# Optimization experiments

Measured on AMD Instinct MI355X. Metric: run time of the kernel, lower is better.

## Reference

```python
import jax, jax.numpy as jnp
import numpy as np

B, C, H = 2, 32, 64  # batch, concat channels, cube side (H==W==D required by attaxis reshapes)
Ch = C // 2


def _conv3d(x, w, b, pad):
    # conv3d block = Conv3d + bias + ReLU (n=1 conv block)
    y = jax.lax.conv_general_dilated(x, w, (1, 1, 1), [(p, p) for p in pad],
                                     dimension_numbers=('NCDHW', 'OIDHW', 'NCDHW'))
    return jax.nn.relu(y + b[None, :, None, None, None])


def setup_inputs():
    key = jax.random.key(0)
    ks = jax.random.split(key, 16)
    w = lambda k, s: jax.random.normal(k, s, dtype=jnp.float32) * 0.05
    z = lambda n: jnp.zeros((n,), jnp.float32)
    return {
        'x1': jax.random.normal(ks[0], (B, Ch, H, H, H), jnp.float32),
        'x2': jax.random.normal(ks[1], (B, Ch, H, H, H), jnp.float32),
        'w_red': w(ks[2], (1, C, 3, 3, 3)), 'b_red': z(1),
        'w_cx': w(ks[3], (1, 1, 1, 1, H)), 'b_cx': z(1),
        'w_cy': w(ks[4], (1, 1, 1, H, 1)), 'b_cy': z(1),
        'w_cz': w(ks[5], (1, 1, H, 1, 1)), 'b_cz': z(1),
        'w_sp1': w(ks[6], (1, 1, 1, 1, 1)), 'b_sp1': z(1),
        'w_sp3': w(ks[7], (1, 1, 3, 3, 3)), 'b_sp3': z(1),
        'w_sp5a': w(ks[8], (1, 1, 3, 3, 3)), 'b_sp5a': z(1),
        'w_sp5b': w(ks[9], (1, 1, 3, 3, 3)), 'b_sp5b': z(1),
        'w_fus': w(ks[10], (C, 1, 3, 3, 3)), 'b_fus': z(C),
        'w_c1': w(ks[11], (Ch, Ch, 3, 3, 3)), 'b_c1': z(Ch),
        'w_c2': w(ks[12], (Ch, Ch, 3, 3, 3)), 'b_c2': z(Ch),
    }


def _kernal(x, w_cx, b_cx, w_cy, b_cy, w_cz, b_cz,
            w_sp1, b_sp1, w_sp3, b_sp3, w_sp5a, b_sp5a, w_sp5b, b_sp5b):
    b, c, h, ww, d = x.shape
    # xyzaxis: axis-collapsing convs, then attaxis attention over S = h*w tokens
    q = _conv3d(x, w_cx, b_cx, (0, 0, 0))                        # [b,1,h,w,1]
    k = jnp.swapaxes(_conv3d(x, w_cy, b_cy, (0, 0, 0)), 3, 4)    # [b,1,h,d,1]
    v = jnp.swapaxes(_conv3d(x, w_cz, b_cz, (0, 0, 0)), 2, 4)    # [b,1,d,w,1]
    S = h * ww
    Q = q.reshape(b, S, 1)
    K = k.reshape(b, S, 1)
    V = v.reshape(b, S, 1)
    qk = jax.nn.softmax(jnp.einsum('bsc,btc->bst', Q, K), axis=-1)  # [b,S,S]
    xyz = jnp.einsum('bst,btc->bsc', qk, V).reshape(b, 1, h, ww, 1)
    # multi-branch convs + full-tensor att(sp1, sp3, sp5)
    sp1 = _conv3d(x, w_sp1, b_sp1, (0, 0, 0))
    sp3 = _conv3d(x, w_sp3, b_sp3, (1, 1, 1))
    sp5 = _conv3d(_conv3d(x, w_sp5a, b_sp5a, (1, 1, 1)), w_sp5b, b_sp5b, (1, 1, 1))
    attn = jnp.matmul(jax.nn.softmax(jnp.matmul(sp1, sp3), axis=-1), sp5)
    return xyz + attn + x  # xyz broadcasts over last dim


def reference(x1, x2, w_red, b_red, w_cx, b_cx, w_cy, b_cy, w_cz, b_cz,
              w_sp1, b_sp1, w_sp3, b_sp3, w_sp5a, b_sp5a, w_sp5b, b_sp5b,
              w_fus, b_fus, w_c1, b_c1, w_c2, b_c2):
    x = jnp.concatenate([x1, x2], axis=1)                 # [B,C,H,H,H]
    hx = _conv3d(x, w_red, b_red, (1, 1, 1))              # DenseSP.reducePool -> 1 channel
    hx = _kernal(hx, w_cx, b_cx, w_cy, b_cy, w_cz, b_cz,
                 w_sp1, b_sp1, w_sp3, b_sp3, w_sp5a, b_sp5a, w_sp5b, b_sp5b)
    sp = jax.nn.sigmoid(_conv3d(hx, w_fus, b_fus, (1, 1, 1)) + x)  # DenseSP output
    x = sp * x + x
    c = x.shape[1] // 2
    y1 = _conv3d(x[:, :c] + x1, w_c1, b_c1, (1, 1, 1))
    y2 = _conv3d(x[:, c:] + x2, w_c2, b_c2, (1, 1, 1))
    return (y1, y2)
```

## Files before the change

kernel.cpp:

```cpp
#include <hip/hip_runtime.h>

#define DEVFN static __device__ __forceinline__

constexpr int HHH = 262144;
constexpr int HH  = 4096;
constexpr int RP  = 19;

typedef __attribute__((ext_vector_type(8))) short short8;
typedef __attribute__((ext_vector_type(4))) float f32x4;

#define OFF_HX   ((size_t)0)
#define OFF_SP3  (OFF_HX   + 2*(size_t)HHH)
#define OFF_SP5A (OFF_SP3  + 2*(size_t)HHH)
#define OFF_SP5B (OFF_SP5A + 2*(size_t)HHH)
#define OFF_HXO  (OFF_SP5B + 2*(size_t)HHH)
#define OFF_Q    (OFF_HXO  + 2*(size_t)HHH)
#define OFF_K    (OFF_Q    + 2*(size_t)HH)
#define OFF_V    (OFF_K    + 2*(size_t)HH)
#define OFF_XYZ  (OFF_V    + 2*(size_t)HH)
#define OFF_KM   (OFF_XYZ  + 2*(size_t)HH)
#define OFF_Z    (OFF_KM   + 16)
#define OFF_WPRE (OFF_Z    + 32*(size_t)HHH)

DEVFN unsigned short f2bf(float f)
{
    unsigned u = __builtin_bit_cast(unsigned, f);
    u += 0x7fffu + ((u >> 16) & 1u);
    return (unsigned short)(u >> 16);
}

DEVFN void stage1800(const float* __restrict__ src, float* __restrict__ tile,
                     int z0, int y0, int x0, int tid)
{
    for (int i = tid; i < 1800; i += 256) {
        int lz = i / 180;
        int r  = i - lz * 180;
        int ly = r / 18;
        int lx = r - ly * 18;
        int gz = z0 - 1 + lz, gy = y0 - 1 + ly, gx = x0 - 1 + lx;
        float v = 0.f;
        if ((unsigned)(gz | gy | gx) < 64u)
            v = src[(gz * 64 + gy) * 64 + gx];
        tile[(lz * 10 + ly) * RP + lx] = v;
    }
}

DEVFN float4 conv27(const float* __restrict__ tile, int tz, int ty, int txg,
                    const float* __restrict__ wc, float4 acc)
{
#pragma unroll
    for (int dz = 0; dz < 3; ++dz) {
#pragma unroll
        for (int dy = 0; dy < 3; ++dy) {
            const float* row = &tile[((tz + dz) * 10 + (ty + dy)) * RP + txg * 4];
            float p0 = row[0], p1 = row[1], p2 = row[2];
            float p3 = row[3], p4 = row[4], p5 = row[5];
            const float* wr = wc + (dz * 3 + dy) * 3;
            float w0 = wr[0], w1 = wr[1], w2 = wr[2];
            acc.x = fmaf(p0, w0, fmaf(p1, w1, fmaf(p2, w2, acc.x)));
            acc.y = fmaf(p1, w0, fmaf(p2, w1, fmaf(p3, w2, acc.y)));
            acc.z = fmaf(p2, w0, fmaf(p3, w1, fmaf(p4, w2, acc.z)));
            acc.w = fmaf(p3, w0, fmaf(p4, w1, fmaf(p5, w2, acc.w)));
        }
    }
    return acc;
}

__global__ __launch_bounds__(256) void k_wprep(
    const float* __restrict__ w1, const float* __restrict__ w2,
    unsigned short* __restrict__ wpre)
{
    int item = blockIdx.x * 256 + threadIdx.x;
    if (item >= 1792) return;
    int half = item / 896;
    int rem  = item - half * 896;
    int t = rem >> 6, lane = rem & 63;
    const float* w = half ? w2 : w1;
    int co = lane & 15, g = lane >> 4;
    int cihalf = g & 1, tapsel = g >> 1;
    int tap = 2 * t + tapsel;
    unsigned v[4] = {0u, 0u, 0u, 0u};
    if (tap < 27) {
#pragma unroll
        for (int p = 0; p < 4; ++p) {
            unsigned short lo = f2bf(w[(co * 16 + cihalf * 8 + 2 * p) * 27 + tap]);
            unsigned short hi = f2bf(w[(co * 16 + cihalf * 8 + 2 * p + 1) * 27 + tap]);
            v[p] = (unsigned)lo | ((unsigned)hi << 16);
        }
    }
    uint4 pk = {v[0], v[1], v[2], v[3]};
    ((uint4*)wpre)[item] = pk;
}

__global__ __launch_bounds__(256) void k_conv_red32(
    const float* __restrict__ x1, const float* __restrict__ x2,
    const float* __restrict__ w, const float* __restrict__ bias,
    float* __restrict__ hx)
{
    __shared__ __align__(16) float buf[3][1140];
    const int tid = threadIdx.x;
    const int tz = tid >> 6, ty = (tid >> 3) & 7, tx2 = tid & 7;
    const int bz = blockIdx.z;
    const int b = bz >> 4, z0 = (bz & 15) * 4;
    const int y0 = blockIdx.y * 8, x0 = blockIdx.x * 16;

    int gofs[5], lidx[5];
    bool inb[5], act[5];
#pragma unroll
    for (int k = 0; k < 5; ++k) {
        int i = tid + k * 256;
        act[k] = (i < 1080);
        inb[k] = false; gofs[k] = 0; lidx[k] = 0;
        if (act[k]) {
            int lz = i / 180, r = i - lz * 180, ly = r / 18, lx = r - ly * 18;
            lidx[k] = (lz * 10 + ly) * RP + lx;
            int gz = z0 - 1 + lz, gy = y0 - 1 + ly, gx = x0 - 1 + lx;
            if ((unsigned)(gz | gy | gx) < 64u) {
                inb[k] = true;
                gofs[k] = (gz * 64 + gy) * 64 + gx;
            }
        }
    }

#define LOADCH(c, rdst)                                                         \
    {                                                                           \
        const float* s_ = ((c) < 16 ? x1 : x2) + (size_t)(b * 16 + ((c) & 15)) * HHH; \
        _Pragma("unroll")                                                       \
        for (int k = 0; k < 5; ++k) rdst[k] = (act[k] && inb[k]) ? s_[gofs[k]] : 0.f; \
    }
#define STORECH(buf_, rsrc)                                                     \
    {                                                                           \
        _Pragma("unroll")                                                       \
        for (int k = 0; k < 5; ++k) if (act[k]) (buf_)[lidx[k]] = rsrc[k];      \
    }

    float rcur[5], rnext[5];
    LOADCH(0, rcur);
    STORECH(buf[0], rcur);
    LOADCH(1, rcur);
    __syncthreads();

    float2 acc = {0.f, 0.f};
    int cur = 0;
    for (int c = 0; c < 32; ++c) {
        if (c + 2 < 32) LOADCH(c + 2, rnext);
        const float* wc = w + c * 27;
        const float* tb = buf[cur];
#pragma unroll
        for (int dz = 0; dz < 3; ++dz) {
#pragma unroll
            for (int dy = 0; dy < 3; ++dy) {
                const float* row = &tb[((tz + dz) * 10 + (ty + dy)) * RP + tx2 * 2];
                float p0 = row[0], p1 = row[1], p2 = row[2], p3 = row[3];
                const float* wr = wc + (dz * 3 + dy) * 3;
                float w0 = wr[0], w1 = wr[1], w2 = wr[2];
                acc.x = fmaf(p0, w0, fmaf(p1, w1, fmaf(p2, w2, acc.x)));
                acc.y = fmaf(p1, w0, fmaf(p2, w1, fmaf(p3, w2, acc.y)));
            }
        }
        int nxt = cur == 2 ? 0 : cur + 1;
        if (c + 1 < 32) {
            STORECH(buf[nxt], rcur);
#pragma unroll
            for (int k = 0; k < 5; ++k) rcur[k] = rnext[k];
        }
        cur = nxt;
        __syncthreads();
    }
#undef LOADCH
#undef STORECH

    float bv = bias[0];
    float2 o = {fmaxf(acc.x + bv, 0.f), fmaxf(acc.y + bv, 0.f)};
    size_t oidx = (size_t)b * HHH + ((size_t)(z0 + tz) * 64 + (y0 + ty)) * 64 + (x0 + tx2 * 2);
    *(float2*)&hx[oidx] = o;
}

__global__ __launch_bounds__(256) void k_conv1ch(
    const float* __restrict__ in, const float* __restrict__ w,
    const float* __restrict__ bias, float* __restrict__ outp)
{
    __shared__ __align__(16) float tile[1900];
    const int tid = threadIdx.x;
    const int tz = tid >> 5, ty = (tid >> 2) & 7, txg = tid & 3;
    const int b  = blockIdx.z >> 3;
    const int z0 = (blockIdx.z & 7) * 8, y0 = blockIdx.y * 8, x0 = blockIdx.x * 16;

    stage1800(in + (size_t)b * HHH, tile, z0, y0, x0, tid);
    __syncthreads();
    float4 acc = {0.f, 0.f, 0.f, 0.f};
    acc = conv27(tile, tz, ty, txg, w, acc);
    float bv = bias[0];
    float4 o = {fmaxf(acc.x + bv, 0.f), fmaxf(acc.y + bv, 0.f),
                fmaxf(acc.z + bv, 0.f), fmaxf(acc.w + bv, 0.f)};
    size_t oidx = (size_t)b * HHH + ((size_t)(z0 + tz) * 64 + (y0 + ty)) * 64 + (x0 + txg * 4);
    *(float4*)&outp[oidx] = o;
}

__global__ __launch_bounds__(256) void k_conv1ch_dual(
    const float* __restrict__ in,
    const float* __restrict__ wa, const float* __restrict__ ba, float* __restrict__ oa,
    const float* __restrict__ wb, const float* __restrict__ bb, float* __restrict__ ob)
{
    __shared__ __align__(16) float tile[1900];
    const int tid = threadIdx.x;
    const int tz = tid >> 5, ty = (tid >> 2) & 7, txg = tid & 3;
    const int b  = blockIdx.z >> 3;
    const int z0 = (blockIdx.z & 7) * 8, y0 = blockIdx.y * 8, x0 = blockIdx.x * 16;

    stage1800(in + (size_t)b * HHH, tile, z0, y0, x0, tid);
    __syncthreads();
    float4 zero = {0.f, 0.f, 0.f, 0.f};
    float4 aA = conv27(tile, tz, ty, txg, wa, zero);
    float4 aB = conv27(tile, tz, ty, txg, wb, zero);
    float bva = ba[0], bvb = bb[0];
    float4 ra = {fmaxf(aA.x + bva, 0.f), fmaxf(aA.y + bva, 0.f),
                 fmaxf(aA.z + bva, 0.f), fmaxf(aA.w + bva, 0.f)};
    float4 rb = {fmaxf(aB.x + bvb, 0.f), fmaxf(aB.y + bvb, 0.f),
                 fmaxf(aB.z + bvb, 0.f), fmaxf(aB.w + bvb, 0.f)};
    size_t oidx = (size_t)b * HHH + ((size_t)(z0 + tz) * 64 + (y0 + ty)) * 64 + (x0 + txg * 4);
    *(float4*)&oa[oidx] = ra;
    *(float4*)&ob[oidx] = rb;
}

__global__ __launch_bounds__(256) void k_qk(
    const float* __restrict__ hx,
    const float* __restrict__ wq, const float* __restrict__ bq,
    const float* __restrict__ wk, const float* __restrict__ bk,
    float* __restrict__ Q, float* __restrict__ K)
{
    const int bi = blockIdx.x;
    const float* src = hx + (size_t)bi * HH;
    const int tid = threadIdx.x;
    const int j = tid >> 2, q = tid & 3;

    float a = 0.f;
    const float4* sv = (const float4*)(src + j * 64 + q * 16);
#pragma unroll
    for (int k = 0; k < 4; ++k) {
        float4 vv = sv[k];
        a = fmaf(vv.x, wq[q * 16 + k * 4 + 0], a);
        a = fmaf(vv.y, wq[q * 16 + k * 4 + 1], a);
        a = fmaf(vv.z, wq[q * 16 + k * 4 + 2], a);
        a = fmaf(vv.w, wq[q * 16 + k * 4 + 3], a);
    }
    a += __shfl_xor(a, 1); a += __shfl_xor(a, 2);

    float c = 0.f;
#pragma unroll
    for (int jj = 0; jj < 16; ++jj)
        c = fmaf(src[(q * 16 + jj) * 64 + j], wk[q * 16 + jj], c);
    c += __shfl_xor(c, 1); c += __shfl_xor(c, 2);

    if (q == 0) {
        Q[(size_t)bi * 64 + j] = fmaxf(a + bq[0], 0.f);
        K[(size_t)bi * 64 + j] = fmaxf(c + bk[0], 0.f);
    }
}

__global__ __launch_bounds__(256) void k_v(
    const float* __restrict__ hx, const float* __restrict__ wv,
    const float* __restrict__ bv, float* __restrict__ V)
{
    const int bt = blockIdx.x;
    const int b = bt >> 6, t = bt & 63;
    const int tid = threadIdx.x;
    const int j = tid >> 2, q = tid & 3;
    const float* src = hx + (size_t)b * HHH + (size_t)j * 64 + t;
    float a = 0.f;
#pragma unroll
    for (int k = 0; k < 16; ++k) {
        int i = q * 16 + k;
        a = fmaf(src[(size_t)i * HH], wv[i], a);
    }
    a += __shfl_xor(a, 1); a += __shfl_xor(a, 2);
    if (q == 0)
        V[(size_t)b * HH + t * 64 + j] = fmaxf(a + bv[0], 0.f);
}

__global__ void k_kmax(const float* __restrict__ K, float* __restrict__ kmax)
{
    __shared__ float red[256];
    int b = blockIdx.x;
    float m = -1e30f;
    for (int u = threadIdx.x; u < 4096; u += 256) m = fmaxf(m, K[b * 4096 + u]);
    red[threadIdx.x] = m;
    __syncthreads();
    for (int s = 128; s > 0; s >>= 1) {
        if (threadIdx.x < s) red[threadIdx.x] = fmaxf(red[threadIdx.x], red[threadIdx.x + s]);
        __syncthreads();
    }
    if (threadIdx.x == 0) kmax[b] = red[0];
}

__global__ __launch_bounds__(256) void k_xyz(
    const float* __restrict__ Q, const float* __restrict__ K,
    const float* __restrict__ V, const float* __restrict__ kmax,
    float* __restrict__ xyz)
{
    __shared__ float pden[4][64];
    __shared__ float pnum[4][64];
    const int b = blockIdx.y;
    const int chunk = blockIdx.x;
    const int lane = threadIdx.x & 63;
    const int wv = __builtin_amdgcn_readfirstlane(threadIdx.x >> 6);
    const int s = chunk * 64 + lane;
    const float qv = Q[b * 4096 + s];
    const float m = qv * kmax[b];
    const float* Kp = K + b * 4096 + wv * 1024;
    const float* Vp = V + b * 4096 + wv * 1024;
    float den = 0.f, num = 0.f;
#pragma unroll 4
    for (int u = 0; u < 1024; ++u) {
        float e = __expf(fmaf(qv, Kp[u], -m));
        den += e;
        num = fmaf(e, Vp[u], num);
    }
    pden[wv][lane] = den;
    pnum[wv][lane] = num;
    __syncthreads();
    if (threadIdx.x < 64) {
        float d = pden[0][lane] + pden[1][lane] + pden[2][lane] + pden[3][lane];
        float n = pnum[0][lane] + pnum[1][lane] + pnum[2][lane] + pnum[3][lane];
        xyz[b * 4096 + s] = n / d;
    }
}

DEVFN void mac16(const float4* __restrict__ base, int vb, float a, float* acc)
{
    float4 q0 = base[vb], q1 = base[vb + 1], q2 = base[vb + 2], q3 = base[vb + 3];
    float qq[16] = {q0.x, q0.y, q0.z, q0.w, q1.x, q1.y, q1.z, q1.w,
                    q2.x, q2.y, q2.z, q2.w, q3.x, q3.y, q3.z, q3.w};
#pragma unroll
    for (int k = 0; k < 16; ++k) acc[k] = fmaf(a, qq[k], acc[k]);
}

__global__ __launch_bounds__(256) void k_attn(
    const float* __restrict__ hx, const float* __restrict__ sp3,
    const float* __restrict__ sp5, const float* __restrict__ xyz,
    const float* __restrict__ w_sp1, const float* __restrict__ b_sp1,
    float* __restrict__ hxo)
{
    __shared__ __align__(16) float s1[64 * 65];
    __shared__ __align__(16) float s3[4096];
    __shared__ __align__(16) float s5[4096];
    const int tid = threadIdx.x;
    const int bi = blockIdx.x;
    const size_t off = (size_t)bi * HH;
    const float w1 = w_sp1[0], bb = b_sp1[0];
    for (int idx = tid; idx < 4096; idx += 256) {
        float hv = hx[off + idx];
        s1[(idx >> 6) * 65 + (idx & 63)] = fmaxf(fmaf(w1, hv, bb), 0.f);
        s3[idx] = sp3[off + idx];
        s5[idx] = sp5[off + idx];
    }
    __syncthreads();
    const int j = tid >> 2, g = tid & 3, t0 = g * 16;
    float m[16];
#pragma unroll
    for (int k = 0; k < 16; ++k) m[k] = 0.f;
    const float4* s3v = (const float4*)s3;
    for (int r = 0; r < 64; ++r) {
        float a = s1[j * 65 + r];
        mac16(s3v, r * 16 + (t0 >> 2), a, m);
    }
    float mx = m[0];
#pragma unroll
    for (int k = 1; k < 16; ++k) mx = fmaxf(mx, m[k]);
    mx = fmaxf(mx, __shfl_xor(mx, 1));
    mx = fmaxf(mx, __shfl_xor(mx, 2));
    float e[16];
    float sum = 0.f;
#pragma unroll
    for (int k = 0; k < 16; ++k) { e[k] = __expf(m[k] - mx); sum += e[k]; }
    sum += __shfl_xor(sum, 1);
    sum += __shfl_xor(sum, 2);
    const float inv = 1.f / sum;
    __syncthreads();
#pragma unroll
    for (int k = 0; k < 16; ++k) s1[j * 65 + t0 + k] = e[k] * inv;
    __syncthreads();
    float acc[16];
#pragma unroll
    for (int k = 0; k < 16; ++k) acc[k] = 0.f;
    const float4* s5v = (const float4*)s5;
    for (int r = 0; r < 64; ++r) {
        float a = s1[j * 65 + r];
        mac16(s5v, r * 16 + (t0 >> 2), a, acc);
    }
    const float xv = xyz[(size_t)(bi >> 6) * HH + (size_t)(bi & 63) * 64 + j];
    const size_t ob = off + (size_t)j * 64 + t0;
#pragma unroll
    for (int k = 0; k < 16; ++k)
        hxo[ob + k] = xv + acc[k] + hx[ob + k];
}

DEVFN float zcalc(float gg, float bf, float xv)
{
    float t = fmaxf(gg + bf, 0.f) + xv;
    float s = 1.f / (1.f + __expf(-t));
    return xv * (s + 2.f);
}

__global__ __launch_bounds__(256) void k_fuse_half(
    const float* __restrict__ hxo, const float* __restrict__ x1,
    const float* __restrict__ x2, const float* __restrict__ w_fus,
    const float* __restrict__ b_fus, unsigned short* __restrict__ Zb)
{
    __shared__ __align__(16) float tile[1900];
    const int tid = threadIdx.x;
    const int tz = tid >> 5, ty = (tid >> 2) & 7, txg = tid & 3;
    const int bz = blockIdx.z;
    const int zt = bz & 7, bh = bz >> 3;
    const int b = bh >> 1, half = bh & 1;
    const int z0 = zt * 8, y0 = blockIdx.y * 8, x0 = blockIdx.x * 16;

    stage1800(hxo + (size_t)b * HHH, tile, z0, y0, x0, tid);
    __syncthreads();

    const size_t vox = ((size_t)(z0 + tz) * 64 + (y0 + ty)) * 64 + (x0 + txg * 4);
    const float* xbase = (half ? x2 : x1) + (size_t)(b * 16) * HHH + vox;
    const float* wbase = w_fus + (half * 16) * 27;
    const float* bbase = b_fus + half * 16;

    unsigned zp[4][8];
#pragma unroll
    for (int cc = 0; cc < 16; ++cc) {
        float4 g = {0.f, 0.f, 0.f, 0.f};
        g = conv27(tile, tz, ty, txg, wbase + cc * 27, g);
        float4 xv = *(const float4*)(xbase + (size_t)cc * HHH);
        float bf = bbase[cc];
        unsigned short z0v = f2bf(zcalc(g.x, bf, xv.x));
        unsigned short z1v = f2bf(zcalc(g.y, bf, xv.y));
        unsigned short z2v = f2bf(zcalc(g.z, bf, xv.z));
        unsigned short z3v = f2bf(zcalc(g.w, bf, xv.w));
        int p = cc >> 1;
        if ((cc & 1) == 0) {
            zp[0][p] = z0v; zp[1][p] = z1v; zp[2][p] = z2v; zp[3][p] = z3v;
        } else {
            zp[0][p] |= (unsigned)z0v << 16; zp[1][p] |= (unsigned)z1v << 16;
            zp[2][p] |= (unsigned)z2v << 16; zp[3][p] |= (unsigned)z3v << 16;
        }
    }
    unsigned short* zo = Zb + ((size_t)bh * HHH + vox) * 16;
#pragma unroll
    for (int v = 0; v < 4; ++v) {
        uint4 lo = {zp[v][0], zp[v][1], zp[v][2], zp[v][3]};
        uint4 hi = {zp[v][4], zp[v][5], zp[v][6], zp[v][7]};
        *(uint4*)(zo + v * 16)     = lo;
        *(uint4*)(zo + v * 16 + 8) = hi;
    }
}

__global__ __launch_bounds__(512) void k_convc_mfma(
    const unsigned short* __restrict__ Zb,
    const unsigned short* __restrict__ wpre,
    const float* __restrict__ b1, const float* __restrict__ b2,
    float* __restrict__ out)
{
    __shared__ __align__(16) unsigned short tile[1800 * 16];
    const int tid = threadIdx.x;
    const int lane = tid & 63;
    const int wvid = tid >> 6;
    const int bz = blockIdx.z;
    const int b = bz >> 4, half = (bz >> 3) & 1, z0 = (bz & 7) * 8;
    const int y0 = blockIdx.y * 8, x0 = blockIdx.x * 16;
    const float* bias = half ? b2 : b1;

    const int g = lane >> 4;
    const int cihalf = g & 1;
    const int tapsel = g >> 1;

    short8 wf[14];
    const short8* wp = (const short8*)wpre + (half * 14) * 64 + lane;
#pragma unroll
    for (int t = 0; t < 14; ++t) wf[t] = wp[t * 64];

    float bfrag[4];
#pragma unroll
    for (int r = 0; r < 4; ++r) bfrag[r] = bias[g * 4 + r];

    const unsigned short* zsrc = Zb + (size_t)(b * 2 + half) * HHH * 16;
    for (int i = tid; i < 3600; i += 512) {
        int pos = i >> 1, h = i & 1;
        int lz = pos / 180;
        int r2 = pos - lz * 180;
        int ly = r2 / 18, lx = r2 - ly * 18;
        int gz = z0 - 1 + lz, gy = y0 - 1 + ly, gx = x0 - 1 + lx;
        uint4 pk = {0u, 0u, 0u, 0u};
        if ((unsigned)(gz | gy | gx) < 64u) {
            size_t gvox = ((size_t)(gz * 64 + gy)) * 64 + gx;
            pk = *(const uint4*)(zsrc + gvox * 16 + h * 8);
        }
        *(uint4*)&tile[pos * 16 + h * 8] = pk;
    }
    __syncthreads();

    int offs[14];
#pragma unroll
    for (int t = 0; t < 14; ++t) {
        int tap = 2 * t + tapsel;
        int tcl = tap < 27 ? tap : 26;
        int dz = tcl / 9, rr = tcl - dz * 9;
        int dy = rr / 3, dx = rr - dy * 3;
        offs[t] = (((dz * 10 + dy) * 18 + dx + (lane & 15)) << 5) + (cihalf << 4);
    }

    const char* tb = (const char*)tile;
    for (int rr = 0; rr < 8; ++rr) {
        int rowid = wvid * 8 + rr;
        int zr = rowid >> 3, yr = rowid & 7;
        int rbase = ((zr * 10 + yr) * 18) << 5;
        f32x4 acc = {0.f, 0.f, 0.f, 0.f};
        f32x4 acc2 = {0.f, 0.f, 0.f, 0.f};
#pragma unroll
        for (int t = 0; t < 14; t += 2) {
            short8 bf0 = *(const short8*)(tb + (rbase + offs[t]));
            acc = __builtin_amdgcn_mfma_f32_16x16x32_bf16(wf[t], bf0, acc, 0, 0, 0);
            short8 bf1 = *(const short8*)(tb + (rbase + offs[t + 1]));
            acc2 = __builtin_amdgcn_mfma_f32_16x16x32_bf16(wf[t + 1], bf1, acc2, 0, 0, 0);
        }
        size_t vox = ((size_t)(z0 + zr) * 64 + (y0 + yr)) * 64 + x0 + (lane & 15);
        float* ob = out + (size_t)half * (2 * 16 * (size_t)HHH) + (size_t)(b * 16) * HHH + vox;
#pragma unroll
        for (int r = 0; r < 4; ++r) {
            float v = acc[r] + acc2[r] + bfrag[r];
            ob[(size_t)(g * 4 + r) * HHH] = fmaxf(v, 0.f);
        }
    }
}

extern "C" void kernel_launch(void* const* d_in, const int* in_sizes, int n_in,
                              void* d_out, int out_size, void* d_ws, size_t ws_size,
                              hipStream_t stream)
{
    const float* x1     = (const float*)d_in[0];
    const float* x2     = (const float*)d_in[1];
    const float* w_red  = (const float*)d_in[2];
    const float* b_red  = (const float*)d_in[3];
    const float* w_cx   = (const float*)d_in[4];
    const float* b_cx   = (const float*)d_in[5];
    const float* w_cy   = (const float*)d_in[6];
    const float* b_cy   = (const float*)d_in[7];
    const float* w_cz   = (const float*)d_in[8];
    const float* b_cz   = (const float*)d_in[9];
    const float* w_sp1  = (const float*)d_in[10];
    const float* b_sp1  = (const float*)d_in[11];
    const float* w_sp3  = (const float*)d_in[12];
    const float* b_sp3  = (const float*)d_in[13];
    const float* w_sp5a = (const float*)d_in[14];
    const float* b_sp5a = (const float*)d_in[15];
    const float* w_sp5b = (const float*)d_in[16];
    const float* b_sp5b = (const float*)d_in[17];
    const float* w_fus  = (const float*)d_in[18];
    const float* b_fus  = (const float*)d_in[19];
    const float* w_c1   = (const float*)d_in[20];
    const float* b_c1   = (const float*)d_in[21];
    const float* w_c2   = (const float*)d_in[22];
    const float* b_c2   = (const float*)d_in[23];

    float* ws  = (float*)d_ws;
    float* out = (float*)d_out;

    float* HX   = ws + OFF_HX;
    float* SP3  = ws + OFF_SP3;
    float* SP5A = ws + OFF_SP5A;
    float* SP5B = ws + OFF_SP5B;
    float* HXO  = ws + OFF_HXO;
    float* Qb   = ws + OFF_Q;
    float* Kb   = ws + OFF_K;
    float* Vb   = ws + OFF_V;
    float* XYZb = ws + OFF_XYZ;
    float* KM   = ws + OFF_KM;
    unsigned short* Zb   = (unsigned short*)(ws + OFF_Z);
    unsigned short* WPRE = (unsigned short*)(ws + OFF_WPRE);

    k_wprep    <<<7, 256, 0, stream>>>(w_c1, w_c2, WPRE);
    k_conv_red32<<<dim3(4, 8, 32), 256, 0, stream>>>(x1, x2, w_red, b_red, HX);
    k_conv1ch_dual<<<dim3(4, 8, 16), 256, 0, stream>>>(HX, w_sp3, b_sp3, SP3,
                                                       w_sp5a, b_sp5a, SP5A);
    k_conv1ch  <<<dim3(4, 8, 16), 256, 0, stream>>>(SP5A, w_sp5b, b_sp5b, SP5B);
    k_qk       <<<128, 256, 0, stream>>>(HX, w_cx, b_cx, w_cy, b_cy, Qb, Kb);
    k_v        <<<128, 256, 0, stream>>>(HX, w_cz, b_cz, Vb);
    k_kmax     <<<2, 256, 0, stream>>>(Kb, KM);
    k_xyz      <<<dim3(64, 2), 256, 0, stream>>>(Qb, Kb, Vb, KM, XYZb);
    k_attn     <<<128, 256, 0, stream>>>(HX, SP3, SP5B, XYZb, w_sp1, b_sp1, HXO);
    k_fuse_half<<<dim3(4, 8, 32), 256, 0, stream>>>(HXO, x1, x2, w_fus, b_fus, Zb);
    k_convc_mfma<<<dim3(4, 8, 32), 512, 0, stream>>>(Zb, WPRE, b_c1, b_c2, out);
}
```

Before: 205.2 us.

## Pad LDS rows to 20 and use vector neighbor loads; enlarge red32 tile

Changes the shared-memory row stride from 19 to 20 floats so each thread can read its 6-wide neighbourhood with float4+float2 loads instead of scalar loads. The 27-tap neighbourhood is now loaded into registers once and reused across the output channels in the fuse and dual convolution kernels. The 32-channel reduction conv now computes 4 outputs per thread over 8-deep z tiles, halving the grid and cutting halo overhead, at the cost of more registers and LDS per block. The stride-20 padding may introduce more LDS bank conflicts than stride 19.

```diff
diff --git a/kernel.cpp b/kernel.cpp
--- a/kernel.cpp
+++ b/kernel.cpp
@@ -4,7 +4,7 @@
 
 constexpr int HHH = 262144;
 constexpr int HH  = 4096;
-constexpr int RP  = 19;
+constexpr int SP  = 20;
 
 typedef __attribute__((ext_vector_type(8))) short short8;
 typedef __attribute__((ext_vector_type(4))) float f32x4;
@@ -29,8 +29,8 @@
     return (unsigned short)(u >> 16);
 }
 
-DEVFN void stage1800(const float* __restrict__ src, float* __restrict__ tile,
-                     int z0, int y0, int x0, int tid)
+DEVFN void stage20(const float* __restrict__ src, float* __restrict__ tile,
+                   int z0, int y0, int x0, int tid)
 {
     for (int i = tid; i < 1800; i += 256) {
         int lz = i / 180;
@@ -41,27 +41,36 @@
         float v = 0.f;
         if ((unsigned)(gz | gy | gx) < 64u)
             v = src[(gz * 64 + gy) * 64 + gx];
-        tile[(lz * 10 + ly) * RP + lx] = v;
-    }
-}
-
-DEVFN float4 conv27(const float* __restrict__ tile, int tz, int ty, int txg,
-                    const float* __restrict__ wc, float4 acc)
+        tile[(lz * 10 + ly) * SP + lx] = v;
+    }
+}
+
+DEVFN void loadnb(const float* __restrict__ tile, int tz, int ty, int txg,
+                  float4* pa, float2* pb)
 {
 #pragma unroll
     for (int dz = 0; dz < 3; ++dz) {
 #pragma unroll
         for (int dy = 0; dy < 3; ++dy) {
-            const float* row = &tile[((tz + dz) * 10 + (ty + dy)) * RP + txg * 4];
-            float p0 = row[0], p1 = row[1], p2 = row[2];
-            float p3 = row[3], p4 = row[4], p5 = row[5];
-            const float* wr = wc + (dz * 3 + dy) * 3;
-            float w0 = wr[0], w1 = wr[1], w2 = wr[2];
-            acc.x = fmaf(p0, w0, fmaf(p1, w1, fmaf(p2, w2, acc.x)));
-            acc.y = fmaf(p1, w0, fmaf(p2, w1, fmaf(p3, w2, acc.y)));
-            acc.z = fmaf(p2, w0, fmaf(p3, w1, fmaf(p4, w2, acc.z)));
-            acc.w = fmaf(p3, w0, fmaf(p4, w1, fmaf(p5, w2, acc.w)));
-        }
+            const float* row = &tile[((tz + dz) * 10 + (ty + dy)) * SP + txg * 4];
+            pa[dz * 3 + dy] = *(const float4*)row;
+            pb[dz * 3 + dy] = *(const float2*)(row + 4);
+        }
+    }
+}
+
+DEVFN float4 conv27r(const float4* pa, const float2* pb,
+                     const float* __restrict__ wc, float4 acc)
+{
+#pragma unroll
+    for (int t = 0; t < 9; ++t) {
+        float w0 = wc[3 * t], w1 = wc[3 * t + 1], w2 = wc[3 * t + 2];
+        float4 p = pa[t];
+        float2 q = pb[t];
+        acc.x = fmaf(p.x, w0, fmaf(p.y, w1, fmaf(p.z, w2, acc.x)));
+        acc.y = fmaf(p.y, w0, fmaf(p.z, w1, fmaf(p.w, w2, acc.y)));
+        acc.z = fmaf(p.z, w0, fmaf(p.w, w1, fmaf(q.x, w2, acc.z)));
+        acc.w = fmaf(p.w, w0, fmaf(q.x, w1, fmaf(q.y, w2, acc.w)));
     }
     return acc;
 }
@@ -97,23 +106,23 @@
     const float* __restrict__ w, const float* __restrict__ bias,
     float* __restrict__ hx)
 {
-    __shared__ __align__(16) float buf[3][1140];
-    const int tid = threadIdx.x;
-    const int tz = tid >> 6, ty = (tid >> 3) & 7, tx2 = tid & 7;
+    __shared__ __align__(16) float buf[3][2000];
+    const int tid = threadIdx.x;
+    const int tz = tid >> 5, ty = (tid >> 2) & 7, txg = tid & 3;
     const int bz = blockIdx.z;
-    const int b = bz >> 4, z0 = (bz & 15) * 4;
+    const int b = bz >> 3, z0 = (bz & 7) * 8;
     const int y0 = blockIdx.y * 8, x0 = blockIdx.x * 16;
 
-    int gofs[5], lidx[5];
-    bool inb[5], act[5];
-#pragma unroll
-    for (int k = 0; k < 5; ++k) {
+    int gofs[8], lidx[8];
+    bool inb[8], act[8];
+#pragma unroll
+    for (int k = 0; k < 8; ++k) {
         int i = tid + k * 256;
-        act[k] = (i < 1080);
+        act[k] = (i < 1800);
         inb[k] = false; gofs[k] = 0; lidx[k] = 0;
         if (act[k]) {
             int lz = i / 180, r = i - lz * 180, ly = r / 18, lx = r - ly * 18;
-            lidx[k] = (lz * 10 + ly) * RP + lx;
+            lidx[k] = (lz * 10 + ly) * SP + lx;
             int gz = z0 - 1 + lz, gy = y0 - 1 + ly, gx = x0 - 1 + lx;
             if ((unsigned)(gz | gy | gx) < 64u) {
                 inb[k] = true;
@@ -126,21 +135,21 @@
     {                                                                           \
         const float* s_ = ((c) < 16 ? x1 : x2) + (size_t)(b * 16 + ((c) & 15)) * HHH; \
         _Pragma("unroll")                                                       \
-        for (int k = 0; k < 5; ++k) rdst[k] = (act[k] && inb[k]) ? s_[gofs[k]] : 0.f; \
+        for (int k = 0; k < 8; ++k) rdst[k] = (act[k] && inb[k]) ? s_[gofs[k]] : 0.f; \
     }
 #define STORECH(buf_, rsrc)                                                     \
     {                                                                           \
         _Pragma("unroll")                                                       \
-        for (int k = 0; k < 5; ++k) if (act[k]) (buf_)[lidx[k]] = rsrc[k];      \
-    }
-
-    float rcur[5], rnext[5];
+        for (int k = 0; k < 8; ++k) if (act[k]) (buf_)[lidx[k]] = rsrc[k];      \
+    }
+
+    float rcur[8], rnext[8];
     LOADCH(0, rcur);
     STORECH(buf[0], rcur);
     LOADCH(1, rcur);
     __syncthreads();
 
-    float2 acc = {0.f, 0.f};
+    float4 acc = {0.f, 0.f, 0.f, 0.f};
     int cur = 0;
     for (int c = 0; c < 32; ++c) {
         if (c + 2 < 32) LOADCH(c + 2, rnext);
@@ -150,19 +159,22 @@
         for (int dz = 0; dz < 3; ++dz) {
 #pragma unroll
             for (int dy = 0; dy < 3; ++dy) {
-                const float* row = &tb[((tz + dz) * 10 + (ty + dy)) * RP + tx2 * 2];
-                float p0 = row[0], p1 = row[1], p2 = row[2], p3 = row[3];
+                const float* row = &tb[((tz + dz) * 10 + (ty + dy)) * SP + txg * 4];
+                float4 p = *(const float4*)row;
+                float2 q = *(const float2*)(row + 4);
                 const float* wr = wc + (dz * 3 + dy) * 3;
                 float w0 = wr[0], w1 = wr[1], w2 = wr[2];
-                acc.x = fmaf(p0, w0, fmaf(p1, w1, fmaf(p2, w2, acc.x)));
-                acc.y = fmaf(p1, w0, fmaf(p2, w1, fmaf(p3, w2, acc.y)));
+                acc.x = fmaf(p.x, w0, fmaf(p.y, w1, fmaf(p.z, w2, acc.x)));
+                acc.y = fmaf(p.y, w0, fmaf(p.z, w1, fmaf(p.w, w2, acc.y)));
+                acc.z = fmaf(p.z, w0, fmaf(p.w, w1, fmaf(q.x, w2, acc.z)));
+                acc.w = fmaf(p.w, w0, fmaf(q.x, w1, fmaf(q.y, w2, acc.w)));
             }
         }
         int nxt = cur == 2 ? 0 : cur + 1;
         if (c + 1 < 32) {
             STORECH(buf[nxt], rcur);
 #pragma unroll
-            for (int k = 0; k < 5; ++k) rcur[k] = rnext[k];
+            for (int k = 0; k < 8; ++k) rcur[k] = rnext[k];
         }
         cur = nxt;
         __syncthreads();
@@ -171,25 +183,28 @@
 #undef STORECH
 
     float bv = bias[0];
-    float2 o = {fmaxf(acc.x + bv, 0.f), fmaxf(acc.y + bv, 0.f)};
-    size_t oidx = (size_t)b * HHH + ((size_t)(z0 + tz) * 64 + (y0 + ty)) * 64 + (x0 + tx2 * 2);
-    *(float2*)&hx[oidx] = o;
+    float4 o = {fmaxf(acc.x + bv, 0.f), fmaxf(acc.y + bv, 0.f),
+                fmaxf(acc.z + bv, 0.f), fmaxf(acc.w + bv, 0.f)};
+    size_t oidx = (size_t)b * HHH + ((size_t)(z0 + tz) * 64 + (y0 + ty)) * 64 + (x0 + txg * 4);
+    *(float4*)&hx[oidx] = o;
 }
 
 __global__ __launch_bounds__(256) void k_conv1ch(
     const float* __restrict__ in, const float* __restrict__ w,
     const float* __restrict__ bias, float* __restrict__ outp)
 {
-    __shared__ __align__(16) float tile[1900];
+    __shared__ __align__(16) float tile[2000];
     const int tid = threadIdx.x;
     const int tz = tid >> 5, ty = (tid >> 2) & 7, txg = tid & 3;
     const int b  = blockIdx.z >> 3;
     const int z0 = (blockIdx.z & 7) * 8, y0 = blockIdx.y * 8, x0 = blockIdx.x * 16;
 
-    stage1800(in + (size_t)b * HHH, tile, z0, y0, x0, tid);
-    __syncthreads();
+    stage20(in + (size_t)b * HHH, tile, z0, y0, x0, tid);
+    __syncthreads();
+    float4 pa[9]; float2 pb[9];
+    loadnb(tile, tz, ty, txg, pa, pb);
     float4 acc = {0.f, 0.f, 0.f, 0.f};
-    acc = conv27(tile, tz, ty, txg, w, acc);
+    acc = conv27r(pa, pb, w, acc);
     float bv = bias[0];
     float4 o = {fmaxf(acc.x + bv, 0.f), fmaxf(acc.y + bv, 0.f),
                 fmaxf(acc.z + bv, 0.f), fmaxf(acc.w + bv, 0.f)};
@@ -202,17 +217,19 @@
     const float* __restrict__ wa, const float* __restrict__ ba, float* __restrict__ oa,
     const float* __restrict__ wb, const float* __restrict__ bb, float* __restrict__ ob)
 {
-    __shared__ __align__(16) float tile[1900];
+    __shared__ __align__(16) float tile[2000];
     const int tid = threadIdx.x;
     const int tz = tid >> 5, ty = (tid >> 2) & 7, txg = tid & 3;
     const int b  = blockIdx.z >> 3;
     const int z0 = (blockIdx.z & 7) * 8, y0 = blockIdx.y * 8, x0 = blockIdx.x * 16;
 
-    stage1800(in + (size_t)b * HHH, tile, z0, y0, x0, tid);
-    __syncthreads();
+    stage20(in + (size_t)b * HHH, tile, z0, y0, x0, tid);
+    __syncthreads();
+    float4 pa[9]; float2 pb[9];
+    loadnb(tile, tz, ty, txg, pa, pb);
     float4 zero = {0.f, 0.f, 0.f, 0.f};
-    float4 aA = conv27(tile, tz, ty, txg, wa, zero);
-    float4 aB = conv27(tile, tz, ty, txg, wb, zero);
+    float4 aA = conv27r(pa, pb, wa, zero);
+    float4 aB = conv27r(pa, pb, wb, zero);
     float bva = ba[0], bvb = bb[0];
     float4 ra = {fmaxf(aA.x + bva, 0.f), fmaxf(aA.y + bva, 0.f),
                  fmaxf(aA.z + bva, 0.f), fmaxf(aA.w + bva, 0.f)};
@@ -407,7 +424,7 @@
     const float* __restrict__ x2, const float* __restrict__ w_fus,
     const float* __restrict__ b_fus, unsigned short* __restrict__ Zb)
 {
-    __shared__ __align__(16) float tile[1900];
+    __shared__ __align__(16) float tile[2000];
     const int tid = threadIdx.x;
     const int tz = tid >> 5, ty = (tid >> 2) & 7, txg = tid & 3;
     const int bz = blockIdx.z;
@@ -415,8 +432,10 @@
     const int b = bh >> 1, half = bh & 1;
     const int z0 = zt * 8, y0 = blockIdx.y * 8, x0 = blockIdx.x * 16;
 
-    stage1800(hxo + (size_t)b * HHH, tile, z0, y0, x0, tid);
-    __syncthreads();
+    stage20(hxo + (size_t)b * HHH, tile, z0, y0, x0, tid);
+    __syncthreads();
+    float4 pa[9]; float2 pb[9];
+    loadnb(tile, tz, ty, txg, pa, pb);
 
     const size_t vox = ((size_t)(z0 + tz) * 64 + (y0 + ty)) * 64 + (x0 + txg * 4);
     const float* xbase = (half ? x2 : x1) + (size_t)(b * 16) * HHH + vox;
@@ -426,8 +445,8 @@
     unsigned zp[4][8];
 #pragma unroll
     for (int cc = 0; cc < 16; ++cc) {
-        float4 g = {0.f, 0.f, 0.f, 0.f};
-        g = conv27(tile, tz, ty, txg, wbase + cc * 27, g);
+        float4 zero = {0.f, 0.f, 0.f, 0.f};
+        float4 g = conv27r(pa, pb, wbase + cc * 27, zero);
         float4 xv = *(const float4*)(xbase + (size_t)cc * HHH);
         float bf = bbase[cc];
         unsigned short z0v = f2bf(zcalc(g.x, bf, xv.x));
@@ -576,7 +595,7 @@
     unsigned short* WPRE = (unsigned short*)(ws + OFF_WPRE);
 
     k_wprep    <<<7, 256, 0, stream>>>(w_c1, w_c2, WPRE);
-    k_conv_red32<<<dim3(4, 8, 32), 256, 0, stream>>>(x1, x2, w_red, b_red, HX);
+    k_conv_red32<<<dim3(4, 8, 16), 256, 0, stream>>>(x1, x2, w_red, b_red, HX);
     k_conv1ch_dual<<<dim3(4, 8, 16), 256, 0, stream>>>(HX, w_sp3, b_sp3, SP3,
                                                        w_sp5a, b_sp5a, SP5A);
     k_conv1ch  <<<dim3(4, 8, 16), 256, 0, stream>>>(SP5A, w_sp5b, b_sp5b, SP5B);
```

Result: no change. 205.1 us (-0.1%).
